# Performance work log

Measured on AMD Instinct MI355X. Metric: run time of the kernel, lower is better.

Reference implementation:

```python
import jax, jax.numpy as jnp
import numpy as np

B, S, D = 1, 2048, 768
NH = 24; QNOPE = 32; QROPE = 16; QHD = QNOPE + QROPE; VHD = 32
QLR = 384; KVLR = 128
PK_HEADS = 4; KDIM = 128; NEXP = 16384; KNN = 8; EDIM = 768
ACT_HID = 24   # SwiGLU(dim=8): int(2*(4*8)/3)=21 -> rounded up to multiple_of=4 -> 24
SHARED_HID = 3072  # expert_dim * n_shared_experts = 768*4
EPS = 1e-5


def rms_norm(x, w):
    return x * jax.lax.rsqrt(jnp.mean(x * x, -1, keepdims=True) + EPS) * w


def swiglu(x, w1, w2, w3):
    return (jax.nn.silu(x @ w1.T) * (x @ w3.T)) @ w2.T


def rope(t, cos, sin):
    # t: (b, s, h, d); cos/sin: (s, d//2); rotate consecutive pairs (matches apply_rope)
    b, s, h, d = t.shape
    tr = t.reshape(b, s, h, d // 2, 2)
    r, i = tr[..., 0], tr[..., 1]
    c = cos[None, :, None, :]
    sn = sin[None, :, None, :]
    return jnp.stack([r * c - i * sn, r * sn + i * c], -1).reshape(b, s, h, d)


def setup_inputs() -> dict:
    key = jax.random.key(0)
    ks = jax.random.split(key, 20)
    rn = lambda k, shp, sc=0.02: jax.random.normal(k, shp, jnp.float32) * sc
    # RoPE tables: cos/sin of pos * inv_freq, dim = qk_rope_head_dim // 2 = 8
    inv = 1.0 / (10000.0 ** (jnp.arange(0, QROPE, 2, dtype=jnp.float32) / QROPE))
    f = jnp.arange(S, dtype=jnp.float32)[:, None] * inv[None, :]
    # causal additive mask (built here; spec fill 'zeros' is a placeholder)
    mask = jnp.where(jnp.tril(jnp.ones((S, S), bool)), 0.0, -1e9).astype(jnp.float32)[None, None]
    kb = float(1.0 / np.sqrt(KDIM))
    return {
        'x': rn(ks[0], (B, S, D), 1.0),
        'norm1_w': jnp.ones((D,), jnp.float32),
        'q_a_w': rn(ks[1], (QLR, D)),
        'q_a_ln_w': jnp.ones((QLR,), jnp.float32),
        'q_b_w': rn(ks[2], (NH * QHD, QLR)),
        'kv_a_w': rn(ks[3], (KVLR + QROPE, D)),
        'kv_a_ln_w': jnp.ones((KVLR,), jnp.float32),
        'kv_b_w': rn(ks[4], (NH * (QNOPE + VHD), KVLR)),
        'o_w': rn(ks[5], (D, NH * VHD)),
        'norm2_w': jnp.ones((D,), jnp.float32),
        'qp_w': rn(ks[6], (PK_HEADS * KDIM, D)),
        'qp_b': jnp.zeros((PK_HEADS * KDIM,), jnp.float32),
        'bn_g': jnp.ones((PK_HEADS * KDIM,), jnp.float32),
        'bn_b': jnp.zeros((PK_HEADS * KDIM,), jnp.float32),
        'keys': jax.random.uniform(ks[7], (PK_HEADS, NEXP, KDIM), jnp.float32, -kb, kb),
        'aw1': rn(ks[8], (ACT_HID, KNN), 0.1),
        'aw2': rn(ks[9], (KNN, ACT_HID), 0.1),
        'aw3': rn(ks[10], (ACT_HID, KNN), 0.1),
        'w_down': rn(ks[11], (NEXP, EDIM)),
        'w_up': rn(ks[12], (NEXP, EDIM)),
        'sw1': rn(ks[13], (SHARED_HID, D)),
        'sw2': rn(ks[14], (D, SHARED_HID)),
        'sw3': rn(ks[15], (SHARED_HID, D)),
        'mask': mask,
        'freqs_cos': jnp.cos(f),
        'freqs_sin': jnp.sin(f),
    }


def reference(x, norm1_w, q_a_w, q_a_ln_w, q_b_w, kv_a_w, kv_a_ln_w, kv_b_w, o_w,
              norm2_w, qp_w, qp_b, bn_g, bn_b, keys, aw1, aw2, aw3, w_down, w_up,
              sw1, sw2, sw3, mask, freqs_cos, freqs_sin):
    b, s, d = x.shape
    # ---- Attention (MLA-style, pre-norm) ----
    h_in = rms_norm(x, norm1_w)
    q = rms_norm(h_in @ q_a_w.T, q_a_ln_w) @ q_b_w.T
    q = q.reshape(b, s, NH, QHD).transpose(0, 2, 1, 3)            # (b, nh, s, 48)
    q_nope, q_pe = q[..., :QNOPE], q[..., QNOPE:]
    ckv = h_in @ kv_a_w.T                                         # (b, s, 144)
    compressed, k_pe = ckv[..., :KVLR], ckv[..., KVLR:]
    kv = (rms_norm(compressed, kv_a_ln_w) @ kv_b_w.T)
    kv = kv.reshape(b, s, NH, QNOPE + VHD).transpose(0, 2, 1, 3)  # (b, nh, s, 64)
    k_nope, v = kv[..., :QNOPE], kv[..., QNOPE:]
    q_pe = rope(q_pe.transpose(0, 2, 1, 3), freqs_cos, freqs_sin).transpose(0, 2, 1, 3)
    k_pe = rope(k_pe[:, :, None, :], freqs_cos, freqs_sin).transpose(0, 2, 1, 3)  # (b,1,s,16)
    q_states = jnp.concatenate([q_nope, q_pe], -1)                # (b, nh, s, 48)
    k_states = jnp.concatenate([k_nope, jnp.broadcast_to(k_pe, (b, NH, s, QROPE))], -1)
    att = jnp.einsum('bhqd,bhkd->bhqk', q_states, k_states) / np.sqrt(QHD).astype(np.float32) + mask
    probs = jax.nn.softmax(att, -1)
    ctx = jnp.einsum('bhqk,bhkd->bhqd', probs, v).transpose(0, 2, 1, 3).reshape(b, s, NH * VHD)
    h = x + ctx @ o_w.T
    # ---- ALL_MOE (product-key memory FFN) ----
    y = rms_norm(h, norm2_w)
    qflat = y.reshape(-1, d) @ qp_w.T + qp_b
    qflat = qflat / np.sqrt(1.0 + EPS).astype(np.float32) * bn_g + bn_b  # BatchNorm1d eval (mu=0, var=1)
    query = qflat.reshape(b * s, PK_HEADS, KDIM)
    sc = jnp.einsum('nhd,hkd->nhk', query, keys)                  # (b*s, heads, n_keys)
    top_s, top_i = jax.lax.top_k(sc, KNN)                         # (b*s, heads, knn)
    w = jax.nn.softmax(top_s, -1).reshape(b, s, PK_HEADS, KNN)
    idx = top_i.reshape(b, s, PK_HEADS, KNN)
    wd = w_down[idx]                                              # (b, s, heads, knn, D)
    wu = w_up[idx]
    z = jnp.einsum('btd,bthkd->bthk', y, wd)
    z = swiglu(z, aw1, aw2, aw3) * w
    moe = jnp.einsum('bthk,bthkd->btd', z, wu) + swiglu(y, sw1, sw2, sw3)
    return h + moe
```

## Files before the change

### kernel.cpp

```cpp
#include <hip/hip_runtime.h>
#include <hip/hip_bf16.h>
#include <hip/hip_fp16.h>

typedef __hip_bfloat16 bf16;

static constexpr int kS    = 2048;
static constexpr int kD    = 768;
static constexpr int kNH   = 24;
static constexpr int kQHD  = 48;
static constexpr int kVHD  = 32;
static constexpr int kQLR  = 384;
static constexpr int kKVLR = 128;
static constexpr int kPKH  = 4;
static constexpr int kNEXP = 16384;
static constexpr int kSH   = 3072;
static constexpr int kCH   = 768;
static constexpr float kEPS = 1e-5f;

__device__ __forceinline__ float b2f(bf16 v) { return __bfloat162float(v); }
__device__ __forceinline__ float silu_f(float x) { return x / (1.0f + expf(-x)); }

__device__ __forceinline__ float ldf(const void* p, size_t i, int m) {
  if (m == 0) return ((const float*)p)[i];
  if (m == 1) return b2f(((const bf16*)p)[i]);
  return __half2float(((const __half*)p)[i]);
}

__global__ void detect_kernel(const unsigned int* __restrict__ w, int* __restrict__ flag) {
  if (threadIdx.x == 0) {
    unsigned int v = w[0];
    flag[0] = (v == 0x3F800000u) ? 0 : ((v == 0x3C003C00u) ? 2 : 1);
  }
}

__global__ __launch_bounds__(256) void fill_kernel(float* __restrict__ out, float v, int n) {
  int i = blockIdx.x * 256 + threadIdx.x;
  if (i < n) out[i] = v;
}

__global__ __launch_bounds__(256) void rms_in_kernel(
    const void* __restrict__ in, const void* __restrict__ w,
    float* __restrict__ out, int cols, const int* __restrict__ dflag) {
  int m = dflag[0];
  int row = blockIdx.x;
  size_t base = (size_t)row * cols;
  __shared__ float red[256];
  float s = 0.f;
  for (int c = threadIdx.x; c < cols; c += 256) { float v = ldf(in, base + c, m); s += v * v; }
  red[threadIdx.x] = s; __syncthreads();
  for (int o = 128; o > 0; o >>= 1) {
    if (threadIdx.x < o) red[threadIdx.x] += red[threadIdx.x + o];
    __syncthreads();
  }
  float scale = rsqrtf(red[0] / cols + kEPS);
  for (int c = threadIdx.x; c < cols; c += 256)
    out[base + c] = ldf(in, base + c, m) * scale * ldf(w, c, m);
}

__global__ __launch_bounds__(256) void rms_f32_kernel(
    const float* __restrict__ in, int istride, const void* __restrict__ w,
    float* __restrict__ out, int cols, const int* __restrict__ dflag) {
  int m = dflag[0];
  int row = blockIdx.x;
  const float* r = in + (size_t)row * istride;
  __shared__ float red[256];
  float s = 0.f;
  for (int c = threadIdx.x; c < cols; c += 256) { float v = r[c]; s += v * v; }
  red[threadIdx.x] = s; __syncthreads();
  for (int o = 128; o > 0; o >>= 1) {
    if (threadIdx.x < o) red[threadIdx.x] += red[threadIdx.x + o];
    __syncthreads();
  }
  float scale = rsqrtf(red[0] / cols + kEPS);
  for (int c = threadIdx.x; c < cols; c += 256)
    out[(size_t)row * cols + c] = r[c] * scale * ldf(w, c, m);
}

template <bool ACC, int DT>
__device__ __forceinline__ void gemm_body(
    const float* __restrict__ A, int lda,
    const void* __restrict__ W, int ldw, int wrow0, int kofs,
    float* __restrict__ C, int ldc, int N, int K,
    float (*As)[68], float (*Ws)[68]) {
  int row0 = blockIdx.y * 64, col0 = blockIdx.x * 64;
  int tid = threadIdx.x;
  int tx = tid & 15, ty = tid >> 4;
  int am = tid >> 3, ak = (tid & 7) * 4;
  int hn = tid >> 2, hk = (tid & 3) * 8;

  float4 ra0, ra1, rw0, rw1;
  uint4 rh;

  auto fetch = [&](int k0) {
    ra0 = *(const float4*)(A + (size_t)(row0 + am) * lda + k0 + ak);
    ra1 = *(const float4*)(A + (size_t)(row0 + am + 32) * lda + k0 + ak);
    if constexpr (DT == 0) {
      const float* Wf = (const float*)W;
      int n0 = col0 + am, n1 = n0 + 32;
      float4 z = make_float4(0.f, 0.f, 0.f, 0.f);
      rw0 = (n0 < N) ? *(const float4*)(Wf + (size_t)(wrow0 + n0) * ldw + kofs + k0 + ak) : z;
      rw1 = (n1 < N) ? *(const float4*)(Wf + (size_t)(wrow0 + n1) * ldw + kofs + k0 + ak) : z;
    } else {
      int n = col0 + hn;
      if (n < N)
        rh = *(const uint4*)((const unsigned short*)W + (size_t)(wrow0 + n) * ldw + kofs + k0 + hk);
      else
        rh = make_uint4(0u, 0u, 0u, 0u);
    }
  };

  auto stage = [&]() {
    As[ak + 0][am] = ra0.x; As[ak + 1][am] = ra0.y;
    As[ak + 2][am] = ra0.z; As[ak + 3][am] = ra0.w;
    As[ak + 0][am + 32] = ra1.x; As[ak + 1][am + 32] = ra1.y;
    As[ak + 2][am + 32] = ra1.z; As[ak + 3][am + 32] = ra1.w;
    if constexpr (DT == 0) {
      Ws[ak + 0][am] = rw0.x; Ws[ak + 1][am] = rw0.y;
      Ws[ak + 2][am] = rw0.z; Ws[ak + 3][am] = rw0.w;
      Ws[ak + 0][am + 32] = rw1.x; Ws[ak + 1][am + 32] = rw1.y;
      Ws[ak + 2][am + 32] = rw1.z; Ws[ak + 3][am + 32] = rw1.w;
    } else if constexpr (DT == 1) {
      unsigned u[4] = {rh.x, rh.y, rh.z, rh.w};
#pragma unroll
      for (int i = 0; i < 4; i++) {
        Ws[hk + 2 * i][hn]     = __uint_as_float(u[i] << 16);
        Ws[hk + 2 * i + 1][hn] = __uint_as_float(u[i] & 0xFFFF0000u);
      }
    } else {
      unsigned u[4] = {rh.x, rh.y, rh.z, rh.w};
#pragma unroll
      for (int i = 0; i < 4; i++) {
        __half2 h2 = *(__half2*)&u[i];
        float2 f = __half22float2(h2);
        Ws[hk + 2 * i][hn]     = f.x;
        Ws[hk + 2 * i + 1][hn] = f.y;
      }
    }
  };

  float acc[4][4] = {};
  auto compute = [&]() {
#pragma unroll
    for (int kk = 0; kk < 32; kk++) {
      float4 a4 = *(const float4*)&As[kk][ty * 4];
      float4 b4 = *(const float4*)&Ws[kk][tx * 4];
      float a[4] = {a4.x, a4.y, a4.z, a4.w};
      float b[4] = {b4.x, b4.y, b4.z, b4.w};
#pragma unroll
      for (int i = 0; i < 4; i++)
#pragma unroll
        for (int j = 0; j < 4; j++) acc[i][j] += a[i] * b[j];
    }
  };

  fetch(0);
  stage();
  __syncthreads();
  for (int k0 = 32; k0 < K; k0 += 32) {
    fetch(k0);
    compute();
    __syncthreads();
    stage();
    __syncthreads();
  }
  compute();

#pragma unroll
  for (int i = 0; i < 4; i++)
#pragma unroll
    for (int j = 0; j < 4; j++) {
      int col = col0 + tx * 4 + j;
      if (col < N) {
        size_t idx = (size_t)(row0 + ty * 4 + i) * ldc + col;
        C[idx] = (ACC ? C[idx] : 0.f) + acc[i][j];
      }
    }
}

template <bool ACC>
__global__ __launch_bounds__(256) void gemm_kernel(
    const float* __restrict__ A, int lda,
    const void* __restrict__ W, int ldw, int wrow0, int kofs,
    float* __restrict__ C, int ldc,
    int M, int N, int K, const int* __restrict__ dflag) {
  __shared__ float As[32][68];
  __shared__ float Ws[32][68];
  int dm = dflag[0];
  if (dm == 1)      gemm_body<ACC, 1>(A, lda, W, ldw, wrow0, kofs, C, ldc, N, K, As, Ws);
  else if (dm == 0) gemm_body<ACC, 0>(A, lda, W, ldw, wrow0, kofs, C, ldc, N, K, As, Ws);
  else              gemm_body<ACC, 2>(A, lda, W, ldw, wrow0, kofs, C, ldc, N, K, As, Ws);
}

__global__ __launch_bounds__(192) void ropeq_kernel(
    float* __restrict__ q, const void* __restrict__ fc, const void* __restrict__ fs,
    const int* __restrict__ dflag) {
  int m = dflag[0];
  int s = blockIdx.x, t = threadIdx.x;
  int h = t >> 3, p = t & 7;
  float c = ldf(fc, s * 8 + p, m), sn = ldf(fs, s * 8 + p, m);
  size_t base = (size_t)s * (kNH * kQHD) + h * kQHD + 32 + 2 * p;
  float r = q[base], im = q[base + 1];
  q[base]     = r * c - im * sn;
  q[base + 1] = r * sn + im * c;
}

__global__ __launch_bounds__(256) void ropek_kernel(
    const float* __restrict__ ckv, const void* __restrict__ fc, const void* __restrict__ fs,
    float* __restrict__ kpe, const int* __restrict__ dflag) {
  int m = dflag[0];
  int i = blockIdx.x * 256 + threadIdx.x;
  if (i >= kS * 8) return;
  int s = i >> 3, p = i & 7;
  float c = ldf(fc, s * 8 + p, m), sn = ldf(fs, s * 8 + p, m);
  float r  = ckv[(size_t)s * 144 + 128 + 2 * p];
  float im = ckv[(size_t)s * 144 + 128 + 2 * p + 1];
  kpe[s * 16 + 2 * p]     = r * c - im * sn;
  kpe[s * 16 + 2 * p + 1] = r * sn + im * c;
}

__global__ __launch_bounds__(256) void attn_kernel(
    const float* __restrict__ q, const float* __restrict__ kv,
    const float* __restrict__ kpe, float* __restrict__ ctx) {
  constexpr int KT = 64;
  __shared__ float Ks[KT][52];
  __shared__ float Vs[KT][36];
  __shared__ float Pt[KT][33];
  __shared__ float Tm[8][32];
  __shared__ float Sm[8][32];
  __shared__ float Ms[32], Ls[32], Fs[32];
  int qt = blockIdx.x, h = blockIdx.y, t = threadIdx.x;
  int qi = t & 31, g = t >> 5;
  int qrow = qt * 32 + qi;

  float qreg[48];
  const float* qp = q + (size_t)qrow * (kNH * kQHD) + h * kQHD;
#pragma unroll
  for (int i = 0; i < 12; i++) {
    float4 v4 = *(const float4*)(qp + 4 * i);
    qreg[4 * i] = v4.x; qreg[4 * i + 1] = v4.y;
    qreg[4 * i + 2] = v4.z; qreg[4 * i + 3] = v4.w;
  }
  if (t < 32) { Ms[t] = -INFINITY; Ls[t] = 0.f; }
  float acc[4] = {0.f, 0.f, 0.f, 0.f};
  const float scale = 0.144337567297406f;
  int nt = (qt * 32 + 32 + KT - 1) / KT;

  int srow = t >> 2, spart = t & 3;
  for (int tile = 0; tile < nt; tile++) {
    int kbase = tile * KT;
    {
      const float* src = kv + (size_t)(kbase + srow) * (kNH * 64) + h * 64 + spart * 16;
      float4 a = ((const float4*)src)[0];
      float4 b = ((const float4*)src)[1];
      float4 c = ((const float4*)src)[2];
      float4 d = ((const float4*)src)[3];
      if (spart < 2) {
        float* dst = &Ks[srow][spart * 16];
        ((float4*)dst)[0] = a; ((float4*)dst)[1] = b;
        ((float4*)dst)[2] = c; ((float4*)dst)[3] = d;
      } else {
        float* dst = &Vs[srow][(spart - 2) * 16];
        ((float4*)dst)[0] = a; ((float4*)dst)[1] = b;
        ((float4*)dst)[2] = c; ((float4*)dst)[3] = d;
      }
      float4 pe = *(const float4*)(kpe + (size_t)(kbase + srow) * 16 + spart * 4);
      *(float4*)&Ks[srow][32 + spart * 4] = pe;
    }
    __syncthreads();

    float s[8]; float lmax = -INFINITY;
    int k0 = g * 8;
#pragma unroll
    for (int kk = 0; kk < 8; kk++) {
      float d = 0.f;
#pragma unroll
      for (int d4 = 0; d4 < 12; d4++) {
        float4 k4 = *(const float4*)&Ks[k0 + kk][4 * d4];
        d += k4.x * qreg[4 * d4];
        d += k4.y * qreg[4 * d4 + 1];
        d += k4.z * qreg[4 * d4 + 2];
        d += k4.w * qreg[4 * d4 + 3];
      }
      d *= scale;
      if (kbase + k0 + kk > qrow) d = -1e9f;
      s[kk] = d;
      lmax = fmaxf(lmax, d);
    }
    Tm[g][qi] = lmax;
    __syncthreads();

    if (t < 32) {
      float tm = Tm[0][t];
#pragma unroll
      for (int gg = 1; gg < 8; gg++) tm = fmaxf(tm, Tm[gg][t]);
      float mo = Ms[t];
      float mn = fmaxf(mo, tm);
      Fs[t] = expf(mo - mn);
      Ms[t] = mn;
    }
    __syncthreads();

    float mq = Ms[qi];
    float psum = 0.f;
#pragma unroll
    for (int kk = 0; kk < 8; kk++) {
      float e = expf(s[kk] - mq);
      Pt[k0 + kk][qi] = e;
      psum += e;
    }
    Sm[g][qi] = psum;
    __syncthreads();

    if (t < 32) {
      float ls = 0.f;
#pragma unroll
      for (int gg = 0; gg < 8; gg++) ls += Sm[gg][t];
      Ls[t] = Ls[t] * Fs[t] + ls;
    }

    float f = Fs[qi];
#pragma unroll
    for (int j = 0; j < 4; j++) acc[j] *= f;
    int vd0 = g * 4;
#pragma unroll 8
    for (int kk = 0; kk < KT; kk++) {
      float p = Pt[kk][qi];
      float4 v4 = *(const float4*)&Vs[kk][vd0];
      acc[0] += p * v4.x; acc[1] += p * v4.y;
      acc[2] += p * v4.z; acc[3] += p * v4.w;
    }
    __syncthreads();
  }
  float inv = 1.f / Ls[qi];
  float* op = ctx + (size_t)qrow * (kNH * kVHD) + h * kVHD + g * 4;
  op[0] = acc[0] * inv; op[1] = acc[1] * inv;
  op[2] = acc[2] * inv; op[3] = acc[3] * inv;
}

__global__ __launch_bounds__(256) void addx_kernel(
    const void* __restrict__ x, const float* __restrict__ o, float* __restrict__ h, int n,
    const int* __restrict__ dflag) {
  int m = dflag[0];
  int i = blockIdx.x * 256 + threadIdx.x;
  if (i < n) h[i] = ldf(x, i, m) + o[i];
}

__global__ __launch_bounds__(256) void bnq_kernel(
    const float* __restrict__ raw, const void* __restrict__ qp_b,
    const void* __restrict__ g, const void* __restrict__ b,
    float* __restrict__ out, int n, const int* __restrict__ dflag) {
  int m = dflag[0];
  int i = blockIdx.x * 256 + threadIdx.x;
  if (i >= n) return;
  int j = i & 511;
  const float invs = 0.9999950000374996f;
  out[i] = (raw[i] + ldf(qp_b, j, m)) * invs * ldf(g, j, m) + ldf(b, j, m);
}

__global__ __launch_bounds__(256) void convert_keys_kernel(
    const void* __restrict__ keys, float* __restrict__ kf, const int* __restrict__ dflag) {
  int m = dflag[0];
  size_t i = ((size_t)blockIdx.x * 256 + threadIdx.x) * 8;
  if (m == 0) {
    const float4* s = (const float4*)((const float*)keys + i);
    float4 a = s[0], b = s[1];
    *(float4*)(kf + i) = a;
    *(float4*)(kf + i + 4) = b;
  } else if (m == 1) {
    uint4 u = *(const uint4*)((const unsigned short*)keys + i);
    unsigned uu[4] = {u.x, u.y, u.z, u.w};
    float o[8];
#pragma unroll
    for (int j = 0; j < 4; j++) {
      o[2 * j]     = __uint_as_float(uu[j] << 16);
      o[2 * j + 1] = __uint_as_float(uu[j] & 0xFFFF0000u);
    }
    *(float4*)(kf + i)     = make_float4(o[0], o[1], o[2], o[3]);
    *(float4*)(kf + i + 4) = make_float4(o[4], o[5], o[6], o[7]);
  } else {
    uint4 u = *(const uint4*)((const unsigned short*)keys + i);
    unsigned uu[4] = {u.x, u.y, u.z, u.w};
    float o[8];
#pragma unroll
    for (int j = 0; j < 4; j++) {
      __half2 h2 = *(__half2*)&uu[j];
      float2 f = __half22float2(h2);
      o[2 * j] = f.x; o[2 * j + 1] = f.y;
    }
    *(float4*)(kf + i)     = make_float4(o[0], o[1], o[2], o[3]);
    *(float4*)(kf + i + 4) = make_float4(o[4], o[5], o[6], o[7]);
  }
}

__device__ __forceinline__ void pk_tail(
    float* tval, int* tidx, int w, int lane, int n, int h, int rblk,
    float* __restrict__ cv, int* __restrict__ ci,
    float (*ldsv)[64][9], int (*ldsi)[64][9]) {
#pragma unroll
  for (int k = 0; k < 8; k++) { ldsv[w][lane][k] = tval[k]; ldsi[w][lane][k] = tidx[k]; }
  __syncthreads();
  if (w == 0) {
#pragma unroll
    for (int ww = 1; ww < 4; ww++) {
#pragma unroll
      for (int k = 0; k < 8; k++) {
        float cs = ldsv[ww][lane][k]; int cidx = ldsi[ww][lane][k];
        if (cs > tval[7]) {
#pragma unroll
          for (int t = 0; t < 8; t++) {
            if (cs > tval[t]) {
              float tv = tval[t]; int ti = tidx[t];
              tval[t] = cs; tidx[t] = cidx;
              cs = tv; cidx = ti;
            }
          }
        }
      }
    }
    size_t base = ((size_t)(n * 4 + h) * 16 + rblk) * 8;
#pragma unroll
    for (int k = 0; k < 8; k++) { cv[base + k] = tval[k]; ci[base + k] = tidx[k]; }
  }
}

__global__ __launch_bounds__(256) void pk_score_f32_kernel(
    const float* __restrict__ query, const float* __restrict__ keysf,
    float* __restrict__ cv, int* __restrict__ ci) {
  __shared__ float ldsv[4][64][9];
  __shared__ int   ldsi[4][64][9];
  int b    = blockIdx.x;
  int w    = threadIdx.x >> 6, lane = threadIdx.x & 63;
  int rblk = b & 15;
  int h    = (b >> 4) & 3;
  int qb   = b >> 6;
  int n    = qb * 64 + lane;
  int r    = rblk * 4 + w;

  float qv[128];
  const float4* qp = (const float4*)(query + (size_t)n * 512 + h * 128);
#pragma unroll
  for (int i = 0; i < 32; i++) {
    float4 t = qp[i];
    qv[4 * i] = t.x; qv[4 * i + 1] = t.y; qv[4 * i + 2] = t.z; qv[4 * i + 3] = t.w;
  }

  float tval[8]; int tidx[8];
#pragma unroll
  for (int k = 0; k < 8; k++) { tval[k] = -INFINITY; tidx[k] = 0x7FFFFFFF; }

  int e0 = r * 256;
  for (int e = 0; e < 256; e++) {
    int eu = __builtin_amdgcn_readfirstlane(e0 + e);
    const float4* row = (const float4*)(keysf + ((size_t)h * kNEXP + eu) * 128);
    float acc = 0.f;
#pragma unroll
    for (int w4 = 0; w4 < 32; w4++) {
      float4 f4 = row[w4];
      acc += f4.x * qv[4 * w4];
      acc += f4.y * qv[4 * w4 + 1];
      acc += f4.z * qv[4 * w4 + 2];
      acc += f4.w * qv[4 * w4 + 3];
    }
    if (acc > tval[7]) {
      float cs = acc; int cidx = eu;
#pragma unroll
      for (int k = 0; k < 8; k++) {
        if (cs > tval[k]) {
          float tv = tval[k]; int ti = tidx[k];
          tval[k] = cs; tidx[k] = cidx;
          cs = tv; cidx = ti;
        }
      }
    }
  }
  pk_tail(tval, tidx, w, lane, n, h, rblk, cv, ci, ldsv, ldsi);
}

template<int M>
__device__ __forceinline__ void pk_score_body(
    const float* __restrict__ query, const void* __restrict__ keys,
    float* __restrict__ cv, int* __restrict__ ci,
    float (*ldsv)[64][9], int (*ldsi)[64][9]) {
  int b    = blockIdx.x;
  int w    = threadIdx.x >> 6, lane = threadIdx.x & 63;
  int rblk = b & 15;
  int h    = (b >> 4) & 3;
  int qb   = b >> 6;
  int n    = qb * 64 + lane;
  int r    = rblk * 4 + w;

  float qv[128];
  const float4* qp = (const float4*)(query + (size_t)n * 512 + h * 128);
#pragma unroll
  for (int i = 0; i < 32; i++) {
    float4 t = qp[i];
    qv[4 * i] = t.x; qv[4 * i + 1] = t.y; qv[4 * i + 2] = t.z; qv[4 * i + 3] = t.w;
  }

  float tval[8]; int tidx[8];
#pragma unroll
  for (int k = 0; k < 8; k++) { tval[k] = -INFINITY; tidx[k] = 0x7FFFFFFF; }

  int e0 = r * 256;
  for (int e = 0; e < 256; e++) {
    int eu = __builtin_amdgcn_readfirstlane(e0 + e);
    float acc = 0.f;
    if constexpr (M == 1) {
      const uint4* row = (const uint4*)((const unsigned*)keys + ((size_t)h * kNEXP + eu) * 64);
#pragma unroll
      for (int w4 = 0; w4 < 16; w4++) {
        uint4 u4 = row[w4];
        unsigned uu[4] = {u4.x, u4.y, u4.z, u4.w};
#pragma unroll
        for (int j = 0; j < 4; j++) {
          float flo = __uint_as_float(uu[j] << 16);
          float fhi = __uint_as_float(uu[j] & 0xFFFF0000u);
          acc += flo * qv[8 * w4 + 2 * j];
          acc += fhi * qv[8 * w4 + 2 * j + 1];
        }
      }
    } else if constexpr (M == 0) {
      const float4* row = (const float4*)((const float*)keys + ((size_t)h * kNEXP + eu) * 128);
#pragma unroll
      for (int w4 = 0; w4 < 32; w4++) {
        float4 f4 = row[w4];
        acc += f4.x * qv[4 * w4];
        acc += f4.y * qv[4 * w4 + 1];
        acc += f4.z * qv[4 * w4 + 2];
        acc += f4.w * qv[4 * w4 + 3];
      }
    } else {
      const uint4* row = (const uint4*)((const unsigned*)keys + ((size_t)h * kNEXP + eu) * 64);
#pragma unroll
      for (int w4 = 0; w4 < 16; w4++) {
        uint4 u4 = row[w4];
        unsigned uu[4] = {u4.x, u4.y, u4.z, u4.w};
#pragma unroll
        for (int j = 0; j < 4; j++) {
          float flo = __half2float(__ushort_as_half((unsigned short)(uu[j] & 0xFFFFu)));
          float fhi = __half2float(__ushort_as_half((unsigned short)(uu[j] >> 16)));
          acc += flo * qv[8 * w4 + 2 * j];
          acc += fhi * qv[8 * w4 + 2 * j + 1];
        }
      }
    }
    if (acc > tval[7]) {
      float cs = acc; int cidx = eu;
#pragma unroll
      for (int k = 0; k < 8; k++) {
        if (cs > tval[k]) {
          float tv = tval[k]; int ti = tidx[k];
          tval[k] = cs; tidx[k] = cidx;
          cs = tv; cidx = ti;
        }
      }
    }
  }
  pk_tail(tval, tidx, w, lane, n, h, rblk, cv, ci, ldsv, ldsi);
}

__global__ __launch_bounds__(256) void pk_score_kernel(
    const float* __restrict__ query, const void* __restrict__ keys,
    float* __restrict__ cv, int* __restrict__ ci, const int* __restrict__ dflag) {
  __shared__ float ldsv[4][64][9];
  __shared__ int   ldsi[4][64][9];
  int m = dflag[0];
  if (m == 1)      pk_score_body<1>(query, keys, cv, ci, ldsv, ldsi);
  else if (m == 0) pk_score_body<0>(query, keys, cv, ci, ldsv, ldsi);
  else             pk_score_body<2>(query, keys, cv, ci, ldsv, ldsi);
}

__global__ __launch_bounds__(256) void pk_merge_kernel(
    const float* __restrict__ cv, const int* __restrict__ ci,
    int* __restrict__ idx_out, float* __restrict__ w_out) {
  int gw   = blockIdx.x * 4 + (threadIdx.x >> 6);
  int lane = threadIdx.x & 63;
  size_t base = (size_t)gw * 128;
  float lv0 = cv[base + lane * 2],     lv1 = cv[base + lane * 2 + 1];
  int   li0 = ci[base + lane * 2],     li1 = ci[base + lane * 2 + 1];
  float wv[8]; int wi[8];
#pragma unroll
  for (int k = 0; k < 8; k++) {
    float bv = lv0; int bi = li0;
    if (lv1 > bv || (lv1 == bv && li1 < bi)) { bv = lv1; bi = li1; }
#pragma unroll
    for (int o = 32; o > 0; o >>= 1) {
      float ov = __shfl_xor(bv, o);
      int   oi = __shfl_xor(bi, o);
      if (ov > bv || (ov == bv && oi < bi)) { bv = ov; bi = oi; }
    }
    wv[k] = bv; wi[k] = bi;
    if (lv0 == bv && li0 == bi) lv0 = -INFINITY;
    if (lv1 == bv && li1 == bi) lv1 = -INFINITY;
  }
  if (lane == 0) {
    float mx = wv[0];
    float e[8]; float ss = 0.f;
#pragma unroll
    for (int k = 0; k < 8; k++) { e[k] = expf(wv[k] - mx); ss += e[k]; }
#pragma unroll
    for (int k = 0; k < 8; k++) {
      idx_out[(size_t)gw * 8 + k] = wi[k];
      w_out[(size_t)gw * 8 + k]   = e[k] / ss;
    }
  }
}

__global__ __launch_bounds__(64) void kz_kernel(
    const float* __restrict__ y, const int* __restrict__ idxb,
    const void* __restrict__ w_down, float* __restrict__ z, const int* __restrict__ dflag) {
  int m = dflag[0];
  int bid = blockIdx.x;
  int n = bid >> 5, e = bid & 31;
  int row = idxb[(size_t)n * 32 + e] & (kNEXP - 1);
  const float* yr = y + (size_t)n * kD;
  size_t wr = (size_t)row * kD;
  float acc = 0.f;
  for (int d = threadIdx.x; d < kD; d += 64) acc += yr[d] * ldf(w_down, wr + d, m);
  for (int o = 32; o > 0; o >>= 1) acc += __shfl_down(acc, o);
  if (threadIdx.x == 0) z[(size_t)n * 32 + e] = acc;
}

__global__ __launch_bounds__(256) void act_kernel(
    const float* __restrict__ z, const float* __restrict__ wsm,
    const void* __restrict__ aw1, const void* __restrict__ aw2, const void* __restrict__ aw3,
    float* __restrict__ z2, const int* __restrict__ dflag) {
  int m = dflag[0];
  int t = blockIdx.x * 256 + threadIdx.x;
  if (t >= kS * kPKH) return;
  const float* zp = z + (size_t)t * 8;
  float zz[8];
#pragma unroll
  for (int k = 0; k < 8; k++) zz[k] = zp[k];
  float u[24];
#pragma unroll
  for (int j = 0; j < 24; j++) {
    float a1 = 0.f, a3 = 0.f;
#pragma unroll
    for (int k = 0; k < 8; k++) {
      a1 += ldf(aw1, j * 8 + k, m) * zz[k];
      a3 += ldf(aw3, j * 8 + k, m) * zz[k];
    }
    u[j] = silu_f(a1) * a3;
  }
#pragma unroll
  for (int k = 0; k < 8; k++) {
    float o = 0.f;
#pragma unroll
    for (int j = 0; j < 24; j++) o += u[j] * ldf(aw2, k * 24 + j, m);
    z2[(size_t)t * 8 + k] = o * wsm[(size_t)t * 8 + k];
  }
}

__global__ __launch_bounds__(256) void moe_kernel(
    const float* __restrict__ z2, const int* __restrict__ idxb,
    const void* __restrict__ w_up, float* __restrict__ moe, const int* __restrict__ dflag) {
  int m = dflag[0];
  int n = blockIdx.x, tid = threadIdx.x;
  __shared__ float zs[32];
  __shared__ int   is[32];
  if (tid < 32) {
    zs[tid] = z2[(size_t)n * 32 + tid];
    is[tid] = idxb[(size_t)n * 32 + tid] & (kNEXP - 1);
  }
  __syncthreads();
  for (int d = tid; d < kD; d += 256) {
    float acc = 0.f;
#pragma unroll 8
    for (int e = 0; e < 32; e++) acc += zs[e] * ldf(w_up, (size_t)is[e] * kD + d, m);
    moe[(size_t)n * kD + d] = acc;
  }
}

__global__ __launch_bounds__(256) void silumul_kernel(
    float* __restrict__ g1, const float* __restrict__ g3, int n) {
  int i = blockIdx.x * 256 + threadIdx.x;
  if (i < n) g1[i] = silu_f(g1[i]) * g3[i];
}

__global__ __launch_bounds__(256) void combine_kernel(
    const float* __restrict__ h, const float* __restrict__ moe,
    float* __restrict__ out, int n) {
  int i = blockIdx.x * 256 + threadIdx.x;
  if (i < n) out[i] = h[i] + moe[i];
}

extern "C" void kernel_launch(void* const* d_in, const int* in_sizes, int n_in,
                              void* d_out, int out_size, void* d_ws, size_t ws_size,
                              hipStream_t stream) {
  float* out = (float*)d_out;
  dim3 b256(256);

  static const long long kExp[26] = {
    (long long)kS * kD, kD,
    (long long)kQLR * kD, kQLR,
    (long long)kNH * kQHD * kQLR,
    (long long)(kKVLR + 16) * kD, kKVLR,
    (long long)kNH * 64 * kKVLR,
    (long long)kD * kNH * kVHD, kD,
    (long long)kPKH * 128 * kD, kPKH * 128, kPKH * 128, kPKH * 128,
    (long long)kPKH * kNEXP * 128,
    24 * 8, 8 * 24, 24 * 8,
    (long long)kNEXP * kD, (long long)kNEXP * kD,
    (long long)kSH * kD, (long long)kD * kSH, (long long)kSH * kD,
    (long long)kS * kS, (long long)kS * 8, (long long)kS * 8,
  };
  int map[26];
  bool used[256] = {};
  bool ok = (n_in >= 26 && n_in <= 256);
  if (ok) {
    for (int j = 0; j < 26; j++) {
      int found = -1;
      for (int i = 0; i < n_in; i++)
        if (!used[i] && (long long)in_sizes[i] == kExp[j]) { found = i; break; }
      if (found < 0) { ok = false; break; }
      used[found] = true;
      map[j] = found;
    }
  }
  if (!ok) {
    fill_kernel<<<(out_size + 255) / 256, b256, 0, stream>>>(out, 100.0f, out_size);
    return;
  }

  const void* x        = d_in[map[0]];
  const void* norm1_w  = d_in[map[1]];
  const void* q_a_w    = d_in[map[2]];
  const void* q_a_ln_w = d_in[map[3]];
  const void* q_b_w    = d_in[map[4]];
  const void* kv_a_w   = d_in[map[5]];
  const void* kv_a_ln_w= d_in[map[6]];
  const void* kv_b_w   = d_in[map[7]];
  const void* o_w      = d_in[map[8]];
  const void* norm2_w  = d_in[map[9]];
  const void* qp_w     = d_in[map[10]];
  const void* qp_b     = d_in[map[11]];
  const void* bn_g     = d_in[map[12]];
  const void* bn_b     = d_in[map[13]];
  const void* keys     = d_in[map[14]];
  const void* aw1      = d_in[map[15]];
  const void* aw2      = d_in[map[16]];
  const void* aw3      = d_in[map[17]];
  const void* w_down   = d_in[map[18]];
  const void* w_up     = d_in[map[19]];
  const void* sw1      = d_in[map[20]];
  const void* sw2      = d_in[map[21]];
  const void* sw3      = d_in[map[22]];
  const void* fcos     = d_in[map[24]];
  const void* fsin     = d_in[map[25]];

  float* ws = (float*)d_ws;
  size_t off = 0;
  auto alloc = [&](size_t n) { float* p = ws + off; off += n; return p; };

  int*   dflag = (int*)alloc(16);
  float* slotA = alloc((size_t)kS * kD);
  float* slotB = alloc((size_t)kS * kQLR);
  float* slotC = alloc((size_t)kS * kNH * kQHD);
  float* ckv   = alloc((size_t)kS * 144);
  float* cn    = alloc((size_t)kS * kKVLR);
  float* kpe   = alloc((size_t)kS * 16);
  float* slotD = alloc((size_t)kS * kNH * 64);
  float* hbuf  = alloc((size_t)kS * kD);
  float* y     = alloc((size_t)kS * kD);
  size_t need_bytes = off * sizeof(float);
  if (ws_size < need_bytes) return;

  size_t nkeys = (size_t)kPKH * kNEXP * 128;
  float* keysf = ws + off;
  bool have_kf = (ws_size >= (off + nkeys) * sizeof(float));

  float* h_in  = slotA;
  float* qa    = slotB;
  float* qan   = hbuf;
  float* q     = slotC;
  float* kv    = slotD;
  float* ctx   = slotA;
  float* otmp  = slotC;
  float* qpraw = slotA;
  float* query = slotD + (size_t)kS * kD;
  int*   idxb  = (int*)slotB;
  float* wsm   = slotB + 65536;
  float* z     = slotB + 2 * 65536;
  float* z2    = slotB + 3 * 65536;
  float* moe   = slotD + (size_t)kS * kD;
  float* g1c   = slotC;
  float* g3c   = slotD;
  float* cand_v = slotA;
  int*   cand_i = (int*)slotC;

  detect_kernel<<<1, 64, 0, stream>>>((const unsigned int*)norm1_w, dflag);
  rms_in_kernel<<<kS, b256, 0, stream>>>(x, norm1_w, h_in, kD, dflag);
  gemm_kernel<false><<<dim3(6, 32), b256, 0, stream>>>(h_in, kD, q_a_w, kD, 0, 0, qa, kQLR, kS, kQLR, kD, dflag);
  rms_f32_kernel<<<kS, b256, 0, stream>>>(qa, kQLR, q_a_ln_w, qan, kQLR, dflag);
  gemm_kernel<false><<<dim3(18, 32), b256, 0, stream>>>(qan, kQLR, q_b_w, kQLR, 0, 0, q, kNH * kQHD, kS, kNH * kQHD, kQLR, dflag);
  gemm_kernel<false><<<dim3(3, 32), b256, 0, stream>>>(h_in, kD, kv_a_w, kD, 0, 0, ckv, 144, kS, 144, kD, dflag);
  rms_f32_kernel<<<kS, b256, 0, stream>>>(ckv, 144, kv_a_ln_w, cn, kKVLR, dflag);
  ropeq_kernel<<<kS, dim3(192), 0, stream>>>(q, fcos, fsin, dflag);
  ropek_kernel<<<(kS * 8 + 255) / 256, b256, 0, stream>>>(ckv, fcos, fsin, kpe, dflag);
  gemm_kernel<false><<<dim3(24, 32), b256, 0, stream>>>(cn, kKVLR, kv_b_w, kKVLR, 0, 0, kv, kNH * 64, kS, kNH * 64, kKVLR, dflag);
  if (have_kf)
    convert_keys_kernel<<<dim3((unsigned)(nkeys / 8 / 256)), b256, 0, stream>>>(keys, keysf, dflag);
  attn_kernel<<<dim3(kS / 32, kNH), b256, 0, stream>>>(q, kv, kpe, ctx);
  gemm_kernel<false><<<dim3(12, 32), b256, 0, stream>>>(ctx, kD, o_w, kD, 0, 0, otmp, kD, kS, kD, kD, dflag);
  addx_kernel<<<(kS * kD + 255) / 256, b256, 0, stream>>>(x, otmp, hbuf, kS * kD, dflag);
  rms_f32_kernel<<<kS, b256, 0, stream>>>(hbuf, kD, norm2_w, y, kD, dflag);
  gemm_kernel<false><<<dim3(8, 32), b256, 0, stream>>>(y, kD, qp_w, kD, 0, 0, qpraw, 512, kS, 512, kD, dflag);
  bnq_kernel<<<(kS * 512 + 255) / 256, b256, 0, stream>>>(qpraw, qp_b, bn_g, bn_b, query, kS * 512, dflag);
  if (have_kf)
    pk_score_f32_kernel<<<dim3(2048), b256, 0, stream>>>(query, keysf, cand_v, cand_i);
  else
    pk_score_kernel<<<dim3(2048), b256, 0, stream>>>(query, keys, cand_v, cand_i, dflag);
  pk_merge_kernel<<<dim3(2048), b256, 0, stream>>>(cand_v, cand_i, idxb, wsm);
  kz_kernel<<<kS * 32, dim3(64), 0, stream>>>(y, idxb, w_down, z, dflag);
  act_kernel<<<(kS * kPKH + 255) / 256, b256, 0, stream>>>(z, wsm, aw1, aw2, aw3, z2, dflag);
  moe_kernel<<<kS, b256, 0, stream>>>(z2, idxb, w_up, moe, dflag);
  for (int c = 0; c < kSH; c += kCH) {
    gemm_kernel<false><<<dim3(12, 32), b256, 0, stream>>>(y, kD, sw1, kD, c, 0, g1c, kCH, kS, kCH, kD, dflag);
    gemm_kernel<false><<<dim3(12, 32), b256, 0, stream>>>(y, kD, sw3, kD, c, 0, g3c, kCH, kS, kCH, kD, dflag);
    silumul_kernel<<<(kS * kCH + 255) / 256, b256, 0, stream>>>(g1c, g3c, kS * kCH);
    gemm_kernel<true><<<dim3(12, 32), b256, 0, stream>>>(g1c, kCH, sw2, kSH, 0, c, moe, kD, kS, kD, kCH, dflag);
  }
  combine_kernel<<<(kS * kD + 255) / 256, b256, 0, stream>>>(hbuf, moe, out, kS * kD);
}
```

Measured before the change: 3.199 ms.

## Stage product-key queries in LDS and score 16 keys per pass

The fp32 product-key scoring kernel now loads the block's 64 queries into shared memory, where before each thread held its 128-float query in registers. The inner loop then computes 16 key dot products at once, reading each query float4 from LDS a single time per 16 keys, and applies the top-8 insertion afterward. The aim is to cut register pressure from the per-thread query array and to give more independent FMA chains and wave-uniform key loads. In exchange it adds LDS traffic, a 32 KB shared buffer reused for the tail, and extra barriers, which may lower occupancy.

```diff
diff --git a/kernel.cpp b/kernel.cpp
--- a/kernel.cpp
+++ b/kernel.cpp
@@ -426,53 +426,69 @@
 __global__ __launch_bounds__(256) void pk_score_f32_kernel(
     const float* __restrict__ query, const float* __restrict__ keysf,
     float* __restrict__ cv, int* __restrict__ ci) {
-  __shared__ float ldsv[4][64][9];
-  __shared__ int   ldsi[4][64][9];
+  __shared__ __align__(16) unsigned char smem[32768];
+  float4 (*Qs4)[64] = (float4 (*)[64])smem;
   int b    = blockIdx.x;
   int w    = threadIdx.x >> 6, lane = threadIdx.x & 63;
   int rblk = b & 15;
   int h    = (b >> 4) & 3;
   int qb   = b >> 6;
-  int n    = qb * 64 + lane;
+  int n0   = qb * 64;
+  int n    = n0 + lane;
   int r    = rblk * 4 + w;
 
-  float qv[128];
-  const float4* qp = (const float4*)(query + (size_t)n * 512 + h * 128);
-#pragma unroll
-  for (int i = 0; i < 32; i++) {
-    float4 t = qp[i];
-    qv[4 * i] = t.x; qv[4 * i + 1] = t.y; qv[4 * i + 2] = t.z; qv[4 * i + 3] = t.w;
-  }
+  {
+    int row = threadIdx.x >> 2, part = threadIdx.x & 3;
+    const float4* src = (const float4*)(query + (size_t)(n0 + row) * 512 + h * 128 + part * 32);
+#pragma unroll
+    for (int j = 0; j < 8; j++) Qs4[part * 8 + j][row] = src[j];
+  }
+  __syncthreads();
 
   float tval[8]; int tidx[8];
 #pragma unroll
   for (int k = 0; k < 8; k++) { tval[k] = -INFINITY; tidx[k] = 0x7FFFFFFF; }
 
+  const float4* hbase = (const float4*)(keysf + (size_t)h * kNEXP * 128);
   int e0 = r * 256;
-  for (int e = 0; e < 256; e++) {
-    int eu = __builtin_amdgcn_readfirstlane(e0 + e);
-    const float4* row = (const float4*)(keysf + ((size_t)h * kNEXP + eu) * 128);
-    float acc = 0.f;
-#pragma unroll
-    for (int w4 = 0; w4 < 32; w4++) {
-      float4 f4 = row[w4];
-      acc += f4.x * qv[4 * w4];
-      acc += f4.y * qv[4 * w4 + 1];
-      acc += f4.z * qv[4 * w4 + 2];
-      acc += f4.w * qv[4 * w4 + 3];
-    }
-    if (acc > tval[7]) {
-      float cs = acc; int cidx = eu;
-#pragma unroll
-      for (int k = 0; k < 8; k++) {
-        if (cs > tval[k]) {
-          float tv = tval[k]; int ti = tidx[k];
-          tval[k] = cs; tidx[k] = cidx;
-          cs = tv; cidx = ti;
+  for (int g = 0; g < 256; g += 16) {
+    int eb = __builtin_amdgcn_readfirstlane(e0 + g);
+    const float4* rows = hbase + (size_t)eb * 32;
+    float acc[16];
+#pragma unroll
+    for (int e = 0; e < 16; e++) acc[e] = 0.f;
+#pragma unroll 8
+    for (int d4 = 0; d4 < 32; d4++) {
+      float4 q4 = Qs4[d4][lane];
+#pragma unroll
+      for (int e = 0; e < 16; e++) {
+        float4 k4 = rows[(size_t)e * 32 + d4];
+        acc[e] += k4.x * q4.x;
+        acc[e] += k4.y * q4.y;
+        acc[e] += k4.z * q4.z;
+        acc[e] += k4.w * q4.w;
+      }
+    }
+#pragma unroll
+    for (int e = 0; e < 16; e++) {
+      float cs = acc[e];
+      if (cs > tval[7]) {
+        int cidx = eb + e;
+#pragma unroll
+        for (int k = 0; k < 8; k++) {
+          if (cs > tval[k]) {
+            float tv = tval[k]; int ti = tidx[k];
+            tval[k] = cs; tidx[k] = cidx;
+            cs = tv; cidx = ti;
+          }
         }
       }
     }
   }
+
+  __syncthreads();
+  float (*ldsv)[64][9] = (float (*)[64][9])smem;
+  int   (*ldsi)[64][9] = (int (*)[64][9])(smem + 9216);
   pk_tail(tval, tidx, w, lane, n, h, rblk, cv, ci, ldsv, ldsi);
 }
 
```

Result: slower. 4.265 ms (+33.3%).
